# Performance work log

Hardware: AMD Instinct MI355X
Metric: run time of the kernel (lower is better)

## Reference

```python
import jax, jax.numpy as jnp
import numpy as np

N_NODES = 100000
N_EDGES = 3200000
N_GRAPHS = 1000
FEAT = 512
EMB = 7
N_CLASSES = 10


def gcn_conv(x, W, b, src, dst, n_nodes):
    # PyG GCNConv: add self-loops, symmetric normalization, aggregate src->dst.
    h = x @ W  # [N, emb] — transform first (emb is tiny)
    loops = jnp.arange(n_nodes, dtype=src.dtype)
    es = jnp.concatenate([src, loops])
    ed = jnp.concatenate([dst, loops])
    deg = jax.ops.segment_sum(jnp.ones_like(ed, dtype=h.dtype), ed, num_segments=n_nodes)
    dinv = jnp.where(deg > 0, jax.lax.rsqrt(deg), 0.0)
    norm = dinv[es] * dinv[ed]  # [E+N]
    msgs = h[es] * norm[:, None]
    out = jax.ops.segment_sum(msgs, ed, num_segments=n_nodes)
    return out + b


def setup_inputs() -> dict:
    key = jax.random.key(0)
    ks = jax.random.split(key, 8)
    x = jax.random.normal(ks[0], (N_NODES, FEAT), dtype=jnp.float32)
    edge_index = jax.random.randint(ks[1], (2, N_EDGES), 0, N_NODES, dtype=jnp.int64)
    batch_index = jnp.sort(jax.random.randint(ks[2], (N_NODES,), 0, N_GRAPHS, dtype=jnp.int64))
    s_in = 1.0 / np.sqrt(FEAT)
    s_h = 1.0 / np.sqrt(EMB)
    W_in = jax.random.uniform(ks[3], (FEAT, EMB), jnp.float32, -s_in, s_in)
    b_in = jnp.zeros((EMB,), jnp.float32)
    W_conv1 = jax.random.uniform(ks[4], (EMB, EMB), jnp.float32, -s_h, s_h)
    b_conv1 = jnp.zeros((EMB,), jnp.float32)
    W_out = jax.random.uniform(ks[5], (EMB, N_CLASSES), jnp.float32, -s_h, s_h)
    b_out = jax.random.uniform(ks[6], (N_CLASSES,), jnp.float32, -s_h, s_h)
    return {"x": x, "edge_index": edge_index, "batch_index": batch_index,
            "W_in": W_in, "b_in": b_in, "W_conv1": W_conv1, "b_conv1": b_conv1,
            "W_out": W_out, "b_out": b_out}


def reference(x, edge_index, batch_index, W_in, b_in, W_conv1, b_conv1, W_out, b_out):
    src, dst = edge_index[0], edge_index[1]
    out = jax.nn.relu(gcn_conv(x, W_in, b_in, src, dst, N_NODES))  # [N, 7]
    # final_conv_acts (computed by the original but NOT used in the returned logits)
    _final_conv_acts = jax.nn.relu(gcn_conv(out, W_conv1, b_conv1, src, dst, N_NODES))
    # global mean pool over batch_index (on `out`, matching the original forward)
    sums = jax.ops.segment_sum(out, batch_index, num_segments=N_GRAPHS)
    counts = jax.ops.segment_sum(jnp.ones((N_NODES,), out.dtype), batch_index, num_segments=N_GRAPHS)
    pooled = sums / jnp.maximum(counts, 1.0)[:, None]  # [G, 7]
    logits = pooled @ W_out + b_out  # [G, classes]
    return jax.nn.softmax(logits, axis=1)
```

## Files before the change

### kernel.cpp

```cpp
#include <hip/hip_runtime.h>

#define N_NODES   100000
#define N_EDGES   3200000
#define N_GRAPHS  1000
#define FEAT      512
#define EMB       7
#define HP        8
#define N_CLASSES 10

#define BSH       8
#define DMASK     255
#define NBUCK     391
#define TCOLS     392
#define NB_A      512
#define TILE_A    6250
#define NIT       25
#define SEGCAP    9216
#define MMF       391
#define GSPAN     16

__device__ __forceinline__ int load_idx(const void* p, long long i, int is32) {
    if (is32) return ((const int*)p)[i];
    return (int)((const long long*)p)[i];
}

__device__ int edge_is32(const void* p) {
    __shared__ int sflag;
    if (threadIdx.x == 0) sflag = 0;
    __syncthreads();
    const int* w = (const int*)p;
    int any = 0;
    for (int k = threadIdx.x; k < 2048; k += blockDim.x)
        if (w[2 * k + 1] != 0) any = 1;
    if (any) atomicOr(&sflag, 1);
    __syncthreads();
    return sflag;
}

__device__ int batch_is32(const void* p) {
    __shared__ int sflag;
    if (threadIdx.x == 0) sflag = 0;
    __syncthreads();
    const int* w = (const int*)p;
    int any = 0;
    for (int k = 1024 + threadIdx.x; k < 2048; k += blockDim.x)
        if (w[2 * k + 1] != 0) any = 1;
    if (any) atomicOr(&sflag, 1);
    __syncthreads();
    return sflag;
}

__device__ void mm_span(int nbase, const float* __restrict__ x,
                        const float* __restrict__ W, float* __restrict__ h) {
    int n = nbase + (int)threadIdx.x;
    if (n >= N_NODES) return;
    const float4* xr = (const float4*)(x + (size_t)n * FEAT);
    float acc[EMB];
#pragma unroll
    for (int j = 0; j < EMB; ++j) acc[j] = 0.0f;
#pragma unroll 4
    for (int k4 = 0; k4 < FEAT / 4; ++k4) {
        float4 v = xr[k4];
        const float* w = W + k4 * 4 * EMB;
#pragma unroll
        for (int j = 0; j < EMB; ++j) {
            float a = acc[j];
            a = fmaf(v.x, w[0 * EMB + j], a);
            a = fmaf(v.y, w[1 * EMB + j], a);
            a = fmaf(v.z, w[2 * EMB + j], a);
            a = fmaf(v.w, w[3 * EMB + j], a);
            acc[j] = a;
        }
    }
    float4* o = (float4*)(h + (size_t)n * HP);
    o[0] = make_float4(acc[0], acc[1], acc[2], acc[3]);
    o[1] = make_float4(acc[4], acc[5], acc[6], 0.0f);
}

__global__ void k_sortblk(const void* __restrict__ eidx, int* __restrict__ T,
                          int* __restrict__ gpk, const float* __restrict__ x,
                          const float* __restrict__ W, float* __restrict__ h) {
    if (blockIdx.x >= NB_A) { mm_span(((int)blockIdx.x - NB_A) * 256, x, W, h); return; }
    __shared__ int stage[TILE_A];
    __shared__ int bins[NBUCK];
    __shared__ int cur[NBUCK];
    __shared__ int pairv[256];
    __shared__ int wsum[4];
    int is32 = edge_is32(eidx);
    const int b = (int)blockIdx.x, t = (int)threadIdx.x;
    for (int k = t; k < NBUCK; k += 256) bins[k] = 0;
    __syncthreads();
    long long e0 = (long long)b * TILE_A;
    int pk[NIT], bk[NIT];
#pragma unroll
    for (int it = 0; it < NIT; ++it) {
        int i = it * 256 + t;
        if (i < TILE_A) {
            int src = load_idx(eidx, e0 + i, is32);
            int d   = load_idx(eidx, (long long)N_EDGES + e0 + i, is32);
            pk[it] = src | ((d & DMASK) << 17);
            bk[it] = d >> BSH;
            atomicAdd(&bins[bk[it]], 1);
        } else { pk[it] = 0; bk[it] = -1; }
    }
    __syncthreads();
    int c0 = (2 * t     < NBUCK) ? bins[2 * t]     : 0;
    int c1 = (2 * t + 1 < NBUCK) ? bins[2 * t + 1] : 0;
    int pr = c0 + c1;
    int inc = pr;
    for (int o = 1; o < 64; o <<= 1) {
        int u = __shfl_up(inc, o);
        if ((t & 63) >= o) inc += u;
    }
    if ((t & 63) == 63) wsum[t >> 6] = inc;
    pairv[t] = inc;
    __syncthreads();
    int add = 0, wv = t >> 6;
    if (wv >= 1) add += wsum[0];
    if (wv >= 2) add += wsum[1];
    if (wv >= 3) add += wsum[2];
    int excl = inc + add - pr;
    __syncthreads();
    if (2 * t     < NBUCK) { bins[2 * t]     = excl;      cur[2 * t]     = excl; }
    if (2 * t + 1 < NBUCK) { bins[2 * t + 1] = excl + c0; cur[2 * t + 1] = excl + c0; }
    __syncthreads();
    for (int k = t; k < NBUCK; k += 256)
        T[b * TCOLS + k] = b * TILE_A + bins[k];
    if (t == 0) T[b * TCOLS + NBUCK] = (b + 1) * TILE_A;
#pragma unroll
    for (int it = 0; it < NIT; ++it) {
        if (bk[it] >= 0) {
            int slot = atomicAdd(&cur[bk[it]], 1);
            stage[slot] = pk[it];
        }
    }
    __syncthreads();
    for (int i = t; i < TILE_A; i += 256)
        gpk[b * TILE_A + i] = stage[i];
}

__device__ int load_runs(const int* __restrict__ T, int k,
                         int* rstart, int* rst, int* wsum) {
    const int t = (int)threadIdx.x;
    int b0 = 2 * t, b1 = 2 * t + 1;
    int s0 = T[b0 * TCOLS + k], e0 = T[b0 * TCOLS + k + 1];
    int s1 = T[b1 * TCOLS + k], e1 = T[b1 * TCOLS + k + 1];
    rstart[b0] = s0; rstart[b1] = s1;
    int c0 = e0 - s0, c1 = e1 - s1;
    int pr = c0 + c1;
    int inc = pr;
    for (int o = 1; o < 64; o <<= 1) {
        int u = __shfl_up(inc, o);
        if ((t & 63) >= o) inc += u;
    }
    if ((t & 63) == 63) wsum[t >> 6] = inc;
    __syncthreads();
    int add = 0, wv = t >> 6;
    if (wv >= 1) add += wsum[0];
    if (wv >= 2) add += wsum[1];
    if (wv >= 3) add += wsum[2];
    int excl = inc + add - pr;
    rst[b0] = excl;
    rst[b1] = excl + c0;
    if (t == 255) rst[512] = excl + pr;
    __syncthreads();
    return rst[512];
}

__device__ __forceinline__ int run_of(const int* rst, int i) {
    int lo = 0, hi = 512;
    while (lo + 1 < hi) { int m = (lo + hi) >> 1; if (rst[m] <= i) lo = m; else hi = m; }
    return lo;
}

__global__ void k_nodecnt(const int* __restrict__ T, const int* __restrict__ gpk,
                          int* __restrict__ cnt, float* __restrict__ h,
                          float* __restrict__ gsum) {
    __shared__ int rstart[512], rst[513], wsum[4];
    __shared__ int bin[256];
    const int k = (int)blockIdx.x, t = (int)threadIdx.x;
    if (k < 32) {
        int idx = k * 256 + t;
        if (idx < N_GRAPHS * 8) gsum[idx] = 0.0f;
    }
    bin[t] = 0;
    int total = load_runs(T, k, rstart, rst, wsum);
    __syncthreads();
    for (int i = t; i < total; i += 256) {
        int b = run_of(rst, i);
        int p = gpk[rstart[b] + (i - rst[b])];
        atomicAdd(&bin[(p >> 17) & DMASK], 1);
    }
    __syncthreads();
    int node = (k << BSH) + t;
    if (node < N_NODES) {
        int c = bin[t];
        cnt[node] = c;
        float di = rsqrtf((float)c + 1.0f);
        float4* hp = (float4*)(h + (size_t)node * HP);
        float4 a = hp[0], cc = hp[1];
        hp[0] = make_float4(a.x * di, a.y * di, a.z * di, a.w * di);
        hp[1] = make_float4(cc.x * di, cc.y * di, cc.z * di, 0.0f);
    }
}

__global__ void k_ggather(const int* __restrict__ T, const int* __restrict__ gpk,
                          const int* __restrict__ cnt, const float* __restrict__ h,
                          const float* __restrict__ b_in, const void* __restrict__ batch,
                          float* __restrict__ gsum) {
    __shared__ int stage[SEGCAP];
    __shared__ int rstart[512], rst[513], wsum[4];
    __shared__ int bin[256], loff[256], curs[256], pairv[256];
    __shared__ float gsl[GSPAN][8];
    __shared__ int gmin_s;
    const int k = (int)blockIdx.x, t = (int)threadIdx.x;
    int bis32 = batch_is32(batch);
    if (t == 0) gmin_s = load_idx(batch, (long long)(k << BSH), bis32);
    if (t < GSPAN * 8) ((float*)gsl)[t] = 0.0f;
    int total = load_runs(T, k, rstart, rst, wsum);
    int len = (total > SEGCAP) ? SEGCAP : total;
    {
        int node = (k << BSH) + t;
        bin[t] = (node < N_NODES) ? cnt[node] : 0;
        curs[t] = 0;
    }
    __syncthreads();
    const int gmin = gmin_s;
    {
        int v = bin[t];
        int inc = v;
        for (int o = 1; o < 64; o <<= 1) {
            int u = __shfl_up(inc, o);
            if ((t & 63) >= o) inc += u;
        }
        pairv[t] = inc;
        __syncthreads();
        int add = 0, wv = t >> 6;
        if (wv >= 1) add += pairv[63];
        if (wv >= 2) add += pairv[127];
        if (wv >= 3) add += pairv[191];
        loff[t] = inc + add - v;
    }
    __syncthreads();
    for (int i = t; i < len; i += 256) {
        int b = run_of(rst, i);
        int p = gpk[rstart[b] + (i - rst[b])];
        int dl = (p >> 17) & DMASK;
        int r = atomicAdd(&curs[dl], 1);
        stage[loff[dl] + r] = p & 0x1FFFF;
    }
    __syncthreads();
    const float4* h4 = (const float4*)h;
    int q = t & 3;
#pragma unroll
    for (int g4 = 0; g4 < 4; ++g4) {
        int nl = (t >> 2) + g4 * 64;
        int node = (k << BSH) + nl;
        if (node < N_NODES) {
            int o = loff[nl], c = bin[nl];
            float acc[EMB];
#pragma unroll
            for (int j = 0; j < EMB; ++j) acc[j] = 0.0f;
            for (int kk = q; kk < c; kk += 4) {
                int s = stage[o + kk];
                float4 a4 = h4[(size_t)s * 2];
                float4 c4 = h4[(size_t)s * 2 + 1];
                acc[0] += a4.x; acc[1] += a4.y; acc[2] += a4.z; acc[3] += a4.w;
                acc[4] += c4.x; acc[5] += c4.y; acc[6] += c4.z;
            }
            if (q == 0) {
                float4 a4 = h4[(size_t)node * 2];
                float4 c4 = h4[(size_t)node * 2 + 1];
                acc[0] += a4.x; acc[1] += a4.y; acc[2] += a4.z; acc[3] += a4.w;
                acc[4] += c4.x; acc[5] += c4.y; acc[6] += c4.z;
            }
#pragma unroll
            for (int j = 0; j < EMB; ++j) {
                acc[j] += __shfl_xor(acc[j], 1);
                acc[j] += __shfl_xor(acc[j], 2);
            }
            float di = rsqrtf((float)c + 1.0f);
            int j0 = 2 * q;
            float v0 = fmaxf(fmaf(di, acc[j0], b_in[j0]), 0.0f);
            float v1 = (j0 + 1 < EMB)
                     ? fmaxf(fmaf(di, acc[j0 + 1], b_in[j0 + 1]), 0.0f) : 0.0f;
            int g = load_idx(batch, node, bis32);
            int gi = g - gmin;
            if (gi < GSPAN) {
                atomicAdd(&gsl[gi][j0], v0);
                atomicAdd(&gsl[gi][j0 + 1], v1);
            } else {
                atomicAdd(&gsum[(size_t)g * 8 + j0], v0);
                atomicAdd(&gsum[(size_t)g * 8 + j0 + 1], v1);
            }
        }
    }
    __syncthreads();
    if (t < GSPAN * 8) {
        int r = t >> 3, c = t & 7;
        float v = gsl[r][c];
        int g = gmin + r;
        if (v != 0.0f && g < N_GRAPHS) atomicAdd(&gsum[(size_t)g * 8 + c], v);
    }
}

__global__ void k_final(const float* __restrict__ gsum, const void* __restrict__ batch,
                        const float* __restrict__ W_out, const float* __restrict__ b_out,
                        float* __restrict__ out) {
    int is32 = batch_is32(batch);
    int g = (int)blockIdx.x * 256 + (int)threadIdx.x;
    if (g >= N_GRAPHS) return;
    int n0, n1;
    {
        int lo = 0, hi = N_NODES;
        while (lo < hi) { int m = (lo + hi) >> 1; if (load_idx(batch, m, is32) < g) lo = m + 1; else hi = m; }
        n0 = lo;
        hi = N_NODES;
        while (lo < hi) { int m = (lo + hi) >> 1; if (load_idx(batch, m, is32) < g + 1) lo = m + 1; else hi = m; }
        n1 = lo;
    }
    float inv = 1.0f / fmaxf((float)(n1 - n0), 1.0f);
    float sums[EMB];
#pragma unroll
    for (int j = 0; j < EMB; ++j) sums[j] = gsum[(size_t)g * 8 + j] * inv;
    float logit[N_CLASSES];
    float mx = -1e30f;
#pragma unroll
    for (int c = 0; c < N_CLASSES; ++c) {
        float l = b_out[c];
#pragma unroll
        for (int j = 0; j < EMB; ++j)
            l = fmaf(sums[j], W_out[j * N_CLASSES + c], l);
        logit[c] = l;
        mx = fmaxf(mx, l);
    }
    float se = 0.0f;
#pragma unroll
    for (int c = 0; c < N_CLASSES; ++c) {
        logit[c] = expf(logit[c] - mx);
        se += logit[c];
    }
    float is = 1.0f / se;
#pragma unroll
    for (int c = 0; c < N_CLASSES; ++c)
        out[(size_t)g * N_CLASSES + c] = logit[c] * is;
}

extern "C" void kernel_launch(void* const* d_in, const int* in_sizes, int n_in,
                              void* d_out, int out_size, void* d_ws, size_t ws_size,
                              hipStream_t stream) {
    const float* x     = (const float*)d_in[0];
    const void*  eidx  = d_in[1];
    const void*  batch = d_in[2];
    const float* W_in  = (const float*)d_in[3];
    const float* b_in  = (const float*)d_in[4];
    const float* W_out = (const float*)d_in[7];
    const float* b_out = (const float*)d_in[8];
    float* out = (float*)d_out;

    int*   gpk  = (int*)d_ws;
    int*   T    = gpk + N_EDGES;
    int*   cnt  = T + NB_A * TCOLS;
    float* h    = (float*)(cnt + N_NODES);
    float* gsum = h + (size_t)N_NODES * HP;

    const int B = 256;
    k_sortblk<<<NB_A + MMF, B, 0, stream>>>(eidx, T, gpk, x, W_in, h);
    k_nodecnt<<<NBUCK, B, 0, stream>>>(T, gpk, cnt, h, gsum);
    k_ggather<<<NBUCK, B, 0, stream>>>(T, gpk, cnt, h, b_in, batch, gsum);
    k_final  <<<(N_GRAPHS + B - 1) / B, B, 0, stream>>>(gsum, batch, W_out, b_out, out);
}
```

Baseline: 165.0 us.

## Split x@W matmul across sort and count kernels, contiguous per-thread edge scans

```diff
diff --git a/kernel.cpp b/kernel.cpp
--- a/kernel.cpp
+++ b/kernel.cpp
@@ -16,8 +16,9 @@
 #define TILE_A    6250
 #define NIT       25
 #define SEGCAP    9216
-#define MMF       391
 #define GSPAN     16
+#define MM_SB     295
+#define MM_NC     96
 
 __device__ __forceinline__ int load_idx(const void* p, long long i, int is32) {
     if (is32) return ((const int*)p)[i];
@@ -174,8 +175,10 @@
 }
 
 __global__ void k_nodecnt(const int* __restrict__ T, const int* __restrict__ gpk,
-                          int* __restrict__ cnt, float* __restrict__ h,
-                          float* __restrict__ gsum) {
+                          int* __restrict__ cnt, float* __restrict__ gsum,
+                          const float* __restrict__ x, const float* __restrict__ W,
+                          float* __restrict__ h) {
+    if (blockIdx.x >= NBUCK) { mm_span((MM_SB + (int)blockIdx.x - NBUCK) * 256, x, W, h); return; }
     __shared__ int rstart[512], rst[513], wsum[4];
     __shared__ int bin[256];
     const int k = (int)blockIdx.x, t = (int)threadIdx.x;
@@ -186,22 +189,22 @@
     bin[t] = 0;
     int total = load_runs(T, k, rstart, rst, wsum);
     __syncthreads();
-    for (int i = t; i < total; i += 256) {
-        int b = run_of(rst, i);
-        int p = gpk[rstart[b] + (i - rst[b])];
-        atomicAdd(&bin[(p >> 17) & DMASK], 1);
+    int chunk = (total + 255) >> 8;
+    int i0 = t * chunk;
+    int i1 = i0 + chunk; if (i1 > total) i1 = total;
+    if (i0 < total) {
+        int cur = run_of(rst, i0);
+        int nxt = rst[cur + 1];
+        int addr = rstart[cur] + (i0 - rst[cur]);
+        for (int i = i0; i < i1; ++i) {
+            while (i >= nxt) { ++cur; addr = rstart[cur] + (i - rst[cur]); nxt = rst[cur + 1]; }
+            int p = gpk[addr++];
+            atomicAdd(&bin[(p >> 17) & DMASK], 1);
+        }
     }
     __syncthreads();
     int node = (k << BSH) + t;
-    if (node < N_NODES) {
-        int c = bin[t];
-        cnt[node] = c;
-        float di = rsqrtf((float)c + 1.0f);
-        float4* hp = (float4*)(h + (size_t)node * HP);
-        float4 a = hp[0], cc = hp[1];
-        hp[0] = make_float4(a.x * di, a.y * di, a.z * di, a.w * di);
-        hp[1] = make_float4(cc.x * di, cc.y * di, cc.z * di, 0.0f);
-    }
+    if (node < N_NODES) cnt[node] = bin[t];
 }
 
 __global__ void k_ggather(const int* __restrict__ T, const int* __restrict__ gpk,
@@ -242,12 +245,20 @@
         loff[t] = inc + add - v;
     }
     __syncthreads();
-    for (int i = t; i < len; i += 256) {
-        int b = run_of(rst, i);
-        int p = gpk[rstart[b] + (i - rst[b])];
-        int dl = (p >> 17) & DMASK;
-        int r = atomicAdd(&curs[dl], 1);
-        stage[loff[dl] + r] = p & 0x1FFFF;
+    int chunk = (len + 255) >> 8;
+    int i0 = t * chunk;
+    int i1 = i0 + chunk; if (i1 > len) i1 = len;
+    if (i0 < len) {
+        int cur = run_of(rst, i0);
+        int nxt = rst[cur + 1];
+        int addr = rstart[cur] + (i0 - rst[cur]);
+        for (int i = i0; i < i1; ++i) {
+            while (i >= nxt) { ++cur; addr = rstart[cur] + (i - rst[cur]); nxt = rst[cur + 1]; }
+            int p = gpk[addr++];
+            int dl = (p >> 17) & DMASK;
+            int r = atomicAdd(&curs[dl], 1);
+            stage[loff[dl] + r] = p & 0x1FFFF;
+        }
     }
     __syncthreads();
     const float4* h4 = (const float4*)h;
@@ -263,23 +274,28 @@
             for (int j = 0; j < EMB; ++j) acc[j] = 0.0f;
             for (int kk = q; kk < c; kk += 4) {
                 int s = stage[o + kk];
+                float f = rsqrtf((float)cnt[s] + 1.0f);
                 float4 a4 = h4[(size_t)s * 2];
                 float4 c4 = h4[(size_t)s * 2 + 1];
-                acc[0] += a4.x; acc[1] += a4.y; acc[2] += a4.z; acc[3] += a4.w;
-                acc[4] += c4.x; acc[5] += c4.y; acc[6] += c4.z;
+                acc[0] = fmaf(a4.x, f, acc[0]); acc[1] = fmaf(a4.y, f, acc[1]);
+                acc[2] = fmaf(a4.z, f, acc[2]); acc[3] = fmaf(a4.w, f, acc[3]);
+                acc[4] = fmaf(c4.x, f, acc[4]); acc[5] = fmaf(c4.y, f, acc[5]);
+                acc[6] = fmaf(c4.z, f, acc[6]);
             }
+            float di = rsqrtf((float)c + 1.0f);
             if (q == 0) {
                 float4 a4 = h4[(size_t)node * 2];
                 float4 c4 = h4[(size_t)node * 2 + 1];
-                acc[0] += a4.x; acc[1] += a4.y; acc[2] += a4.z; acc[3] += a4.w;
-                acc[4] += c4.x; acc[5] += c4.y; acc[6] += c4.z;
+                acc[0] = fmaf(a4.x, di, acc[0]); acc[1] = fmaf(a4.y, di, acc[1]);
+                acc[2] = fmaf(a4.z, di, acc[2]); acc[3] = fmaf(a4.w, di, acc[3]);
+                acc[4] = fmaf(c4.x, di, acc[4]); acc[5] = fmaf(c4.y, di, acc[5]);
+                acc[6] = fmaf(c4.z, di, acc[6]);
             }
 #pragma unroll
             for (int j = 0; j < EMB; ++j) {
                 acc[j] += __shfl_xor(acc[j], 1);
                 acc[j] += __shfl_xor(acc[j], 2);
             }
-            float di = rsqrtf((float)c + 1.0f);
             int j0 = 2 * q;
             float v0 = fmaxf(fmaf(di, acc[j0], b_in[j0]), 0.0f);
             float v1 = (j0 + 1 < EMB)
@@ -365,8 +381,8 @@
     float* gsum = h + (size_t)N_NODES * HP;
 
     const int B = 256;
-    k_sortblk<<<NB_A + MMF, B, 0, stream>>>(eidx, T, gpk, x, W_in, h);
-    k_nodecnt<<<NBUCK, B, 0, stream>>>(T, gpk, cnt, h, gsum);
+    k_sortblk<<<NB_A + MM_SB, B, 0, stream>>>(eidx, T, gpk, x, W_in, h);
+    k_nodecnt<<<NBUCK + MM_NC, B, 0, stream>>>(T, gpk, cnt, gsum, x, W_in, h);
     k_ggather<<<NBUCK, B, 0, stream>>>(T, gpk, cnt, h, b_in, batch, gsum);
     k_final  <<<(N_GRAPHS + B - 1) / B, B, 0, stream>>>(gsum, batch, W_out, b_out, out);
 }
```

After: 157.8 us (median of 2 runs). -4.4%, faster.
